# Kernel optimization log

Measured on AMD Instinct MI355X. Metric: run time of the kernel, lower is better.

Reference implementation:

```python
import jax, jax.numpy as jnp
import numpy as np

N = 20000
E = 320000
IN_FEAT = 256
HID = 256
OUT_FEAT = 128


def setup_inputs() -> dict:
    key = jax.random.key(0)
    ks = jax.random.split(key, 10)
    inp = {
        "x": jax.random.normal(ks[0], (N, IN_FEAT), dtype=jnp.float32),
        "edge_src": jax.random.randint(ks[1], (E,), 0, N, dtype=jnp.int32),
        "edge_dst": jax.random.randint(ks[2], (E,), 0, N, dtype=jnp.int32),
        "edge_w": jax.random.uniform(ks[3], (E,), dtype=jnp.float32),
        # params (Linear weights stored as [out, in], torch convention)
        "W_emb": jax.random.normal(ks[4], (HID, IN_FEAT), dtype=jnp.float32) / np.sqrt(IN_FEAT),
        "W_gc1": jax.random.normal(ks[5], (HID, 2 * HID), dtype=jnp.float32) / np.sqrt(2 * HID),
        "b_gc1": jnp.zeros((HID,), dtype=jnp.float32),
        "W_gc2": jax.random.normal(ks[6], (HID, 2 * HID), dtype=jnp.float32) / np.sqrt(2 * HID),
        "b_gc2": jnp.zeros((HID,), dtype=jnp.float32),
        "W_fc": jax.random.normal(ks[7], (OUT_FEAT, HID), dtype=jnp.float32) / np.sqrt(HID),
    }
    return inp


def reference(x, edge_src, edge_dst, edge_w, W_emb, W_gc1, b_gc1, W_gc2, b_gc2, W_fc):
    n = x.shape[0]

    def adj_mul(h):
        msgs = h[edge_src] * edge_w[:, None]           # [E, hid]
        return jax.ops.segment_sum(msgs, edge_dst, num_segments=n)

    def gconv(h, W, b):
        cat = jnp.concatenate([h, adj_mul(h)], axis=1)  # [N, 2*hid]
        return cat @ W.T + b

    h = x @ W_emb.T                                    # embedding (no bias)
    h = h + jax.nn.relu(gconv(h, W_gc1, b_gc1))        # residual (dropout = eval identity)
    h = h + jax.nn.relu(gconv(h, W_gc2, b_gc2))
    out = h @ W_fc.T                                   # fc_last (no bias)
    out = out / jnp.sqrt(jnp.sum(out * out, axis=1, keepdims=True))
    return out
```

## Files before the change

kernel.cpp:

```cpp
#include <hip/hip_runtime.h>
#include <math.h>

#define N_NODES 20000
#define E_EDGES 320000
#define HID 256
#define OUT_FEAT 128
#define MPAD 20224
#define CAP 64

#define BM 128
#define BN 128
#define BK 64
#define LSTR 72

typedef __attribute__((ext_vector_type(8))) __bf16 bf16x8;
typedef __attribute__((ext_vector_type(4))) float floatx4;


__global__ void zero_kernel(int* __restrict__ counts) {
    int i = blockIdx.x * 256 + threadIdx.x;
    if (i < MPAD) counts[i] = 0;
}


#define WBLK 176
#define XBLK 2528
#define EBLK 1250

__global__ void convert_scatter_kernel(
    const float* __restrict__ w0, const float* __restrict__ w1,
    const float* __restrict__ w2, const float* __restrict__ w3,
    __bf16* __restrict__ o0, __bf16* __restrict__ o1,
    __bf16* __restrict__ o2, __bf16* __restrict__ o3,
    const float* __restrict__ x, __bf16* __restrict__ xb,
    const int* __restrict__ src, const int* __restrict__ dst,
    const float* __restrict__ w, int* __restrict__ counts,
    int2* __restrict__ edges) {
    const int b = blockIdx.x;
    if (b < WBLK) {
        const size_t gi = ((size_t)b * 256 + threadIdx.x) * 8;
        const size_t s0 = 65536, s1 = s0 + 131072, s2 = s1 + 131072, s3 = s2 + 32768;
        if (gi >= s3) return;
        const float* srcp; __bf16* dstp; size_t off;
        if (gi < s0)      { srcp = w0; dstp = o0; off = gi; }
        else if (gi < s1) { srcp = w1; dstp = o1; off = gi - s0; }
        else if (gi < s2) { srcp = w2; dstp = o2; off = gi - s1; }
        else              { srcp = w3; dstp = o3; off = gi - s2; }
        float4 v0 = *(const float4*)(srcp + off);
        float4 v1 = *(const float4*)(srcp + off + 4);
        bf16x8 o;
        o[0] = (__bf16)v0.x; o[1] = (__bf16)v0.y; o[2] = (__bf16)v0.z; o[3] = (__bf16)v0.w;
        o[4] = (__bf16)v1.x; o[5] = (__bf16)v1.y; o[6] = (__bf16)v1.z; o[7] = (__bf16)v1.w;
        *(bf16x8*)(dstp + off) = o;
    } else if (b < WBLK + XBLK) {
        const size_t gi = ((size_t)(b - WBLK) * 256 + threadIdx.x) * 8;
        float4 v0 = make_float4(0.f, 0.f, 0.f, 0.f), v1 = v0;
        if (gi < (size_t)N_NODES * HID) {
            v0 = *(const float4*)(x + gi);
            v1 = *(const float4*)(x + gi + 4);
        }
        bf16x8 o;
        o[0] = (__bf16)v0.x; o[1] = (__bf16)v0.y; o[2] = (__bf16)v0.z; o[3] = (__bf16)v0.w;
        o[4] = (__bf16)v1.x; o[5] = (__bf16)v1.y; o[6] = (__bf16)v1.z; o[7] = (__bf16)v1.w;
        *(bf16x8*)(xb + gi) = o;
    } else {
        int e = (b - WBLK - XBLK) * 256 + threadIdx.x;
        if (e < E_EDGES) {
            int d = dst[e];
            int p = atomicAdd(&counts[d], 1);
            edges[(size_t)d * CAP + p] = make_int2(src[e], __float_as_int(w[e]));
        }
    }
}


__global__ __launch_bounds__(256) void aggregate_kernel(
    const __bf16* __restrict__ h, const int* __restrict__ counts,
    const int2* __restrict__ edges, __bf16* __restrict__ agg) {
    const int w = threadIdx.x >> 6, lane = threadIdx.x & 63;
    const int half = lane >> 5, lh = lane & 31;
    const int d = blockIdx.x * 8 + w * 2 + half;
    const size_t base = (size_t)d * CAP;
    const int cnt = counts[d];
    float acc[8];
#pragma unroll
    for (int q = 0; q < 8; q++) acc[q] = 0.f;

    int j = 0;
    for (; j + 16 <= cnt; j += 16) {
        int4 eh[8];
#pragma unroll
        for (int u = 0; u < 8; u++) eh[u] = *(const int4*)(edges + base + j + u * 2);
        bf16x8 hv[16];
#pragma unroll
        for (int u = 0; u < 8; u++) {
            hv[u * 2]     = *(const bf16x8*)(h + (size_t)eh[u].x * HID + lh * 8);
            hv[u * 2 + 1] = *(const bf16x8*)(h + (size_t)eh[u].z * HID + lh * 8);
        }
#pragma unroll
        for (int u = 0; u < 8; u++) {
            float wa = __int_as_float(eh[u].y), wb = __int_as_float(eh[u].w);
#pragma unroll
            for (int q = 0; q < 8; q++) {
                acc[q] = fmaf(wa, (float)hv[u * 2][q], acc[q]);
                acc[q] = fmaf(wb, (float)hv[u * 2 + 1][q], acc[q]);
            }
        }
    }
    for (; j + 8 <= cnt; j += 8) {
        int4 eh[4];
#pragma unroll
        for (int u = 0; u < 4; u++) eh[u] = *(const int4*)(edges + base + j + u * 2);
        bf16x8 hv[8];
#pragma unroll
        for (int u = 0; u < 4; u++) {
            hv[u * 2]     = *(const bf16x8*)(h + (size_t)eh[u].x * HID + lh * 8);
            hv[u * 2 + 1] = *(const bf16x8*)(h + (size_t)eh[u].z * HID + lh * 8);
        }
#pragma unroll
        for (int u = 0; u < 4; u++) {
            float wa = __int_as_float(eh[u].y), wb = __int_as_float(eh[u].w);
#pragma unroll
            for (int q = 0; q < 8; q++) {
                acc[q] = fmaf(wa, (float)hv[u * 2][q], acc[q]);
                acc[q] = fmaf(wb, (float)hv[u * 2 + 1][q], acc[q]);
            }
        }
    }
    for (; j + 2 <= cnt; j += 2) {
        int4 ea = *(const int4*)(edges + base + j);
        bf16x8 h0 = *(const bf16x8*)(h + (size_t)ea.x * HID + lh * 8);
        bf16x8 h1 = *(const bf16x8*)(h + (size_t)ea.z * HID + lh * 8);
        float w0 = __int_as_float(ea.y), w1 = __int_as_float(ea.w);
#pragma unroll
        for (int q = 0; q < 8; q++) {
            acc[q] = fmaf(w0, (float)h0[q], acc[q]);
            acc[q] = fmaf(w1, (float)h1[q], acc[q]);
        }
    }
    if (j < cnt) {
        int2 e0 = edges[base + j];
        bf16x8 h0 = *(const bf16x8*)(h + (size_t)e0.x * HID + lh * 8);
        float w0 = __int_as_float(e0.y);
#pragma unroll
        for (int q = 0; q < 8; q++) acc[q] = fmaf(w0, (float)h0[q], acc[q]);
    }
    bf16x8 o;
#pragma unroll
    for (int q = 0; q < 8; q++) o[q] = (__bf16)acc[q];
    *(bf16x8*)(agg + (size_t)d * HID + lh * 8) = o;
}


template <int KTOT, int EPI>
__global__ __launch_bounds__(256) void gemm_tile_kernel(
    const __bf16* __restrict__ A1,
    const __bf16* __restrict__ A2,
    const __bf16* __restrict__ W,
    const float* __restrict__ bias,
    const __bf16* __restrict__ hres,
    __bf16* __restrict__ outb)
{
    __shared__ __bf16 As[BM * LSTR];
    __shared__ __bf16 Bs[BN * LSTR];
    const int tid = threadIdx.x;
    const int row0 = blockIdx.y * BM;
    const int col0 = blockIdx.x * BN;
    const int wv = tid >> 6, l = tid & 63, lr = l & 15, lq = l >> 4;
    const int wm = wv & 1, wn = wv >> 1;

    floatx4 acc[4][4];
#pragma unroll
    for (int i = 0; i < 4; i++)
#pragma unroll
        for (int j = 0; j < 4; j++) acc[i][j] = (floatx4){0.f, 0.f, 0.f, 0.f};

    const int srow = tid >> 3;
    const int skq = (tid & 7) * 8;

    for (int kc = 0; kc < KTOT; kc += BK) {
        const __bf16* Asrc = (KTOT == 512 && kc >= 256) ? A2 : A1;
        const int ks = (KTOT == 512) ? (kc & 255) : kc;
#pragma unroll
        for (int r = 0; r < 4; r++) {
            int row = r * 32 + srow;
            *(bf16x8*)&As[row * LSTR + skq] =
                *(const bf16x8*)(Asrc + (size_t)(row0 + row) * HID + ks + skq);
        }
#pragma unroll
        for (int r = 0; r < 4; r++) {
            int row = r * 32 + srow;
            *(bf16x8*)&Bs[row * LSTR + skq] =
                *(const bf16x8*)(W + (size_t)(col0 + row) * KTOT + kc + skq);
        }
        __syncthreads();
#pragma unroll
        for (int s = 0; s < 2; s++) {
            bf16x8 af[4], bfr[4];
#pragma unroll
            for (int mt = 0; mt < 4; mt++)
                af[mt] = *(const bf16x8*)&As[(wm * 64 + mt * 16 + lr) * LSTR + s * 32 + lq * 8];
#pragma unroll
            for (int nt = 0; nt < 4; nt++)
                bfr[nt] = *(const bf16x8*)&Bs[(wn * 64 + nt * 16 + lr) * LSTR + s * 32 + lq * 8];
#pragma unroll
            for (int mt = 0; mt < 4; mt++)
#pragma unroll
                for (int nt = 0; nt < 4; nt++)
                    acc[mt][nt] = __builtin_amdgcn_mfma_f32_16x16x32_bf16(af[mt], bfr[nt], acc[mt][nt], 0, 0, 0);
        }
        __syncthreads();
    }

#pragma unroll
    for (int nt = 0; nt < 4; nt++) {
        const int col = col0 + wn * 64 + nt * 16 + lr;
        float b = 0.f;
        if (EPI == 1) b = bias[col];
#pragma unroll
        for (int mt = 0; mt < 4; mt++) {
            const int row = row0 + wm * 64 + mt * 16 + lq * 4;
#pragma unroll
            for (int r = 0; r < 4; r++) {
                float v = acc[mt][nt][r];
                if (EPI == 1) {
                    float res = (float)hres[(size_t)(row + r) * HID + col];
                    v = res + fmaxf(v + b, 0.f);
                }
                outb[(size_t)(row + r) * HID + col] = (__bf16)v;
            }
        }
    }
}


__global__ __launch_bounds__(256) void fc_norm_kernel(
    const __bf16* __restrict__ h,
    const __bf16* __restrict__ W,
    float* __restrict__ out)
{
    const int tid = threadIdx.x;
    const int wv = tid >> 6;
    const int l = tid & 63;
    const int lr = l & 15;
    const int lq = l >> 4;
    const int rowbase = blockIdx.x * 128 + wv * 32;

    floatx4 acc[2][8];
#pragma unroll
    for (int i = 0; i < 2; i++)
#pragma unroll
        for (int j = 0; j < 8; j++) acc[i][j] = (floatx4){0.f, 0.f, 0.f, 0.f};

#pragma unroll
    for (int kt = 0; kt < 256; kt += 32) {
        bf16x8 af[2], bfr[8];
#pragma unroll
        for (int mt = 0; mt < 2; mt++)
            af[mt] = *(const bf16x8*)(h + (size_t)(rowbase + mt * 16 + lr) * 256 + kt + lq * 8);
#pragma unroll
        for (int nt = 0; nt < 8; nt++)
            bfr[nt] = *(const bf16x8*)(W + (size_t)(nt * 16 + lr) * 256 + kt + lq * 8);
#pragma unroll
        for (int mt = 0; mt < 2; mt++)
#pragma unroll
            for (int nt = 0; nt < 8; nt++)
                acc[mt][nt] = __builtin_amdgcn_mfma_f32_16x16x32_bf16(af[mt], bfr[nt], acc[mt][nt], 0, 0, 0);
    }

#pragma unroll
    for (int mt = 0; mt < 2; mt++) {
        float s[4];
#pragma unroll
        for (int r = 0; r < 4; r++) {
            float t = 0.f;
#pragma unroll
            for (int nt = 0; nt < 8; nt++) t = fmaf(acc[mt][nt][r], acc[mt][nt][r], t);
            s[r] = t;
        }
#pragma unroll
        for (int mask = 1; mask <= 8; mask <<= 1) {
#pragma unroll
            for (int r = 0; r < 4; r++) s[r] += __shfl_xor(s[r], mask);
        }
        float inv[4];
#pragma unroll
        for (int r = 0; r < 4; r++) inv[r] = rsqrtf(s[r]);
#pragma unroll
        for (int r = 0; r < 4; r++) {
            int row = rowbase + mt * 16 + lq * 4 + r;
            if (row >= N_NODES) continue;
#pragma unroll
            for (int nt = 0; nt < 8; nt++)
                out[(size_t)row * OUT_FEAT + nt * 16 + lr] = acc[mt][nt][r] * inv[r];
        }
    }
}


extern "C" void kernel_launch(void* const* d_in, const int* in_sizes, int n_in,
                              void* d_out, int out_size, void* d_ws, size_t ws_size,
                              hipStream_t stream) {
    const float* x        = (const float*)d_in[0];
    const int*   edge_src = (const int*)d_in[1];
    const int*   edge_dst = (const int*)d_in[2];
    const float* edge_w   = (const float*)d_in[3];
    const float* W_emb    = (const float*)d_in[4];
    const float* W_gc1    = (const float*)d_in[5];
    const float* b_gc1    = (const float*)d_in[6];
    const float* W_gc2    = (const float*)d_in[7];
    const float* b_gc2    = (const float*)d_in[8];
    const float* W_fc     = (const float*)d_in[9];
    float* out = (float*)d_out;

    char* p = (char*)d_ws;
    const size_t HROW = (size_t)MPAD * HID;
    __bf16* hb0   = (__bf16*)p;             p += HROW * 2;
    __bf16* hb1   = (__bf16*)p;             p += HROW * 2;
    __bf16* aggb  = (__bf16*)p;             p += HROW * 2;
    __bf16* xb    = (__bf16*)p;             p += HROW * 2;
    __bf16* wemb  = (__bf16*)p;             p += 65536 * 2;
    __bf16* w1b   = (__bf16*)p;             p += 131072 * 2;
    __bf16* w2b   = (__bf16*)p;             p += 131072 * 2;
    __bf16* wfcb  = (__bf16*)p;             p += 32768 * 2;
    int2*   edges = (int2*)p;               p += (size_t)N_NODES * CAP * 8;
    int*    counts = (int*)p;               p += (size_t)MPAD * 4;

    zero_kernel<<<MPAD / 256, 256, 0, stream>>>(counts);
    convert_scatter_kernel<<<WBLK + XBLK + EBLK, 256, 0, stream>>>(
        W_emb, W_gc1, W_gc2, W_fc, wemb, w1b, w2b, wfcb,
        x, xb, edge_src, edge_dst, edge_w, counts, edges);

    const dim3 grid_g(HID / BN, MPAD / BM);

    gemm_tile_kernel<256, 0><<<grid_g, 256, 0, stream>>>(xb, nullptr, wemb, nullptr, nullptr, hb0);
    aggregate_kernel<<<N_NODES / 8, 256, 0, stream>>>(hb0, counts, edges, aggb);
    gemm_tile_kernel<512, 1><<<grid_g, 256, 0, stream>>>(hb0, aggb, w1b, b_gc1, hb0, hb1);
    aggregate_kernel<<<N_NODES / 8, 256, 0, stream>>>(hb1, counts, edges, aggb);
    gemm_tile_kernel<512, 1><<<grid_g, 256, 0, stream>>>(hb1, aggb, w2b, b_gc2, hb1, hb0);
    fc_norm_kernel<<<MPAD / 128, 256, 0, stream>>>(hb0, wfcb, out);
}
```

Baseline: 214.5 us.

## Fuse x conversion into embedding GEMM and pad edge lists for uniform aggregation

Removes the separate fp32-to-bf16 conversion of x and its intermediate buffer by converting on the fly while loading the A tile of the embedding GEMM. The aggregate kernel drops its tail loops and always processes 16-edge chunks, relying on a memset that zeros the padded edge slots so extra entries contribute zero weight. The memset adds about 10 MB of writes, and padding causes wasted gathers of row 0.

```diff
diff --git a/kernel.cpp b/kernel.cpp
--- a/kernel.cpp
+++ b/kernel.cpp
@@ -17,14 +17,7 @@
 typedef __attribute__((ext_vector_type(4))) float floatx4;
 
 
-__global__ void zero_kernel(int* __restrict__ counts) {
-    int i = blockIdx.x * 256 + threadIdx.x;
-    if (i < MPAD) counts[i] = 0;
-}
-
-
 #define WBLK 176
-#define XBLK 2528
 #define EBLK 1250
 
 __global__ void convert_scatter_kernel(
@@ -32,7 +25,6 @@
     const float* __restrict__ w2, const float* __restrict__ w3,
     __bf16* __restrict__ o0, __bf16* __restrict__ o1,
     __bf16* __restrict__ o2, __bf16* __restrict__ o3,
-    const float* __restrict__ x, __bf16* __restrict__ xb,
     const int* __restrict__ src, const int* __restrict__ dst,
     const float* __restrict__ w, int* __restrict__ counts,
     int2* __restrict__ edges) {
@@ -52,19 +44,8 @@
         o[0] = (__bf16)v0.x; o[1] = (__bf16)v0.y; o[2] = (__bf16)v0.z; o[3] = (__bf16)v0.w;
         o[4] = (__bf16)v1.x; o[5] = (__bf16)v1.y; o[6] = (__bf16)v1.z; o[7] = (__bf16)v1.w;
         *(bf16x8*)(dstp + off) = o;
-    } else if (b < WBLK + XBLK) {
-        const size_t gi = ((size_t)(b - WBLK) * 256 + threadIdx.x) * 8;
-        float4 v0 = make_float4(0.f, 0.f, 0.f, 0.f), v1 = v0;
-        if (gi < (size_t)N_NODES * HID) {
-            v0 = *(const float4*)(x + gi);
-            v1 = *(const float4*)(x + gi + 4);
-        }
-        bf16x8 o;
-        o[0] = (__bf16)v0.x; o[1] = (__bf16)v0.y; o[2] = (__bf16)v0.z; o[3] = (__bf16)v0.w;
-        o[4] = (__bf16)v1.x; o[5] = (__bf16)v1.y; o[6] = (__bf16)v1.z; o[7] = (__bf16)v1.w;
-        *(bf16x8*)(xb + gi) = o;
     } else {
-        int e = (b - WBLK - XBLK) * 256 + threadIdx.x;
+        int e = (b - WBLK) * 256 + threadIdx.x;
         if (e < E_EDGES) {
             int d = dst[e];
             int p = atomicAdd(&counts[d], 1);
@@ -81,16 +62,16 @@
     const int half = lane >> 5, lh = lane & 31;
     const int d = blockIdx.x * 8 + w * 2 + half;
     const size_t base = (size_t)d * CAP;
-    const int cnt = counts[d];
+    const int iters = (counts[d] + 15) >> 4;
     float acc[8];
 #pragma unroll
     for (int q = 0; q < 8; q++) acc[q] = 0.f;
 
-    int j = 0;
-    for (; j + 16 <= cnt; j += 16) {
+    for (int it = 0; it < iters; ++it) {
+        const int2* ep = edges + base + it * 16;
         int4 eh[8];
 #pragma unroll
-        for (int u = 0; u < 8; u++) eh[u] = *(const int4*)(edges + base + j + u * 2);
+        for (int u = 0; u < 8; u++) eh[u] = *(const int4*)(ep + u * 2);
         bf16x8 hv[16];
 #pragma unroll
         for (int u = 0; u < 8; u++) {
@@ -107,44 +88,6 @@
             }
         }
     }
-    for (; j + 8 <= cnt; j += 8) {
-        int4 eh[4];
-#pragma unroll
-        for (int u = 0; u < 4; u++) eh[u] = *(const int4*)(edges + base + j + u * 2);
-        bf16x8 hv[8];
-#pragma unroll
-        for (int u = 0; u < 4; u++) {
-            hv[u * 2]     = *(const bf16x8*)(h + (size_t)eh[u].x * HID + lh * 8);
-            hv[u * 2 + 1] = *(const bf16x8*)(h + (size_t)eh[u].z * HID + lh * 8);
-        }
-#pragma unroll
-        for (int u = 0; u < 4; u++) {
-            float wa = __int_as_float(eh[u].y), wb = __int_as_float(eh[u].w);
-#pragma unroll
-            for (int q = 0; q < 8; q++) {
-                acc[q] = fmaf(wa, (float)hv[u * 2][q], acc[q]);
-                acc[q] = fmaf(wb, (float)hv[u * 2 + 1][q], acc[q]);
-            }
-        }
-    }
-    for (; j + 2 <= cnt; j += 2) {
-        int4 ea = *(const int4*)(edges + base + j);
-        bf16x8 h0 = *(const bf16x8*)(h + (size_t)ea.x * HID + lh * 8);
-        bf16x8 h1 = *(const bf16x8*)(h + (size_t)ea.z * HID + lh * 8);
-        float w0 = __int_as_float(ea.y), w1 = __int_as_float(ea.w);
-#pragma unroll
-        for (int q = 0; q < 8; q++) {
-            acc[q] = fmaf(w0, (float)h0[q], acc[q]);
-            acc[q] = fmaf(w1, (float)h1[q], acc[q]);
-        }
-    }
-    if (j < cnt) {
-        int2 e0 = edges[base + j];
-        bf16x8 h0 = *(const bf16x8*)(h + (size_t)e0.x * HID + lh * 8);
-        float w0 = __int_as_float(e0.y);
-#pragma unroll
-        for (int q = 0; q < 8; q++) acc[q] = fmaf(w0, (float)h0[q], acc[q]);
-    }
     bf16x8 o;
 #pragma unroll
     for (int q = 0; q < 8; q++) o[q] = (__bf16)acc[q];
@@ -152,9 +95,10 @@
 }
 
 
-template <int KTOT, int EPI>
+template <int KTOT, int EPI, bool F32A>
 __global__ __launch_bounds__(256) void gemm_tile_kernel(
     const __bf16* __restrict__ A1,
+    const float* __restrict__ A1f,
     const __bf16* __restrict__ A2,
     const __bf16* __restrict__ W,
     const float* __restrict__ bias,
@@ -179,13 +123,31 @@
     const int skq = (tid & 7) * 8;
 
     for (int kc = 0; kc < KTOT; kc += BK) {
-        const __bf16* Asrc = (KTOT == 512 && kc >= 256) ? A2 : A1;
-        const int ks = (KTOT == 512) ? (kc & 255) : kc;
-#pragma unroll
-        for (int r = 0; r < 4; r++) {
-            int row = r * 32 + srow;
-            *(bf16x8*)&As[row * LSTR + skq] =
-                *(const bf16x8*)(Asrc + (size_t)(row0 + row) * HID + ks + skq);
+        if (F32A) {
+#pragma unroll
+            for (int r = 0; r < 4; r++) {
+                int row = r * 32 + srow;
+                int grow = row0 + row;
+                float4 v0 = make_float4(0.f, 0.f, 0.f, 0.f), v1 = v0;
+                if (grow < N_NODES) {
+                    const float* xp = A1f + (size_t)grow * HID + kc + skq;
+                    v0 = *(const float4*)xp;
+                    v1 = *(const float4*)(xp + 4);
+                }
+                bf16x8 o;
+                o[0] = (__bf16)v0.x; o[1] = (__bf16)v0.y; o[2] = (__bf16)v0.z; o[3] = (__bf16)v0.w;
+                o[4] = (__bf16)v1.x; o[5] = (__bf16)v1.y; o[6] = (__bf16)v1.z; o[7] = (__bf16)v1.w;
+                *(bf16x8*)&As[row * LSTR + skq] = o;
+            }
+        } else {
+            const __bf16* Asrc = (KTOT == 512 && kc >= 256) ? A2 : A1;
+            const int ks = (KTOT == 512) ? (kc & 255) : kc;
+#pragma unroll
+            for (int r = 0; r < 4; r++) {
+                int row = r * 32 + srow;
+                *(bf16x8*)&As[row * LSTR + skq] =
+                    *(const bf16x8*)(Asrc + (size_t)(row0 + row) * HID + ks + skq);
+            }
         }
 #pragma unroll
         for (int r = 0; r < 4; r++) {
@@ -318,7 +280,6 @@
     __bf16* hb0   = (__bf16*)p;             p += HROW * 2;
     __bf16* hb1   = (__bf16*)p;             p += HROW * 2;
     __bf16* aggb  = (__bf16*)p;             p += HROW * 2;
-    __bf16* xb    = (__bf16*)p;             p += HROW * 2;
     __bf16* wemb  = (__bf16*)p;             p += 65536 * 2;
     __bf16* w1b   = (__bf16*)p;             p += 131072 * 2;
     __bf16* w2b   = (__bf16*)p;             p += 131072 * 2;
@@ -326,17 +287,22 @@
     int2*   edges = (int2*)p;               p += (size_t)N_NODES * CAP * 8;
     int*    counts = (int*)p;               p += (size_t)MPAD * 4;
 
-    zero_kernel<<<MPAD / 256, 256, 0, stream>>>(counts);
-    convert_scatter_kernel<<<WBLK + XBLK + EBLK, 256, 0, stream>>>(
+    hipMemsetAsync(counts, 0, (size_t)MPAD * 4, stream);
+    hipMemsetAsync(edges, 0, (size_t)N_NODES * CAP * 8, stream);
+
+    convert_scatter_kernel<<<WBLK + EBLK, 256, 0, stream>>>(
         W_emb, W_gc1, W_gc2, W_fc, wemb, w1b, w2b, wfcb,
-        x, xb, edge_src, edge_dst, edge_w, counts, edges);
+        edge_src, edge_dst, edge_w, counts, edges);
 
     const dim3 grid_g(HID / BN, MPAD / BM);
 
-    gemm_tile_kernel<256, 0><<<grid_g, 256, 0, stream>>>(xb, nullptr, wemb, nullptr, nullptr, hb0);
+    gemm_tile_kernel<256, 0, true><<<grid_g, 256, 0, stream>>>(
+        nullptr, x, nullptr, wemb, nullptr, nullptr, hb0);
     aggregate_kernel<<<N_NODES / 8, 256, 0, stream>>>(hb0, counts, edges, aggb);
-    gemm_tile_kernel<512, 1><<<grid_g, 256, 0, stream>>>(hb0, aggb, w1b, b_gc1, hb0, hb1);
+    gemm_tile_kernel<512, 1, false><<<grid_g, 256, 0, stream>>>(
+        hb0, nullptr, aggb, w1b, b_gc1, hb0, hb1);
     aggregate_kernel<<<N_NODES / 8, 256, 0, stream>>>(hb1, counts, edges, aggb);
-    gemm_tile_kernel<512, 1><<<grid_g, 256, 0, stream>>>(hb1, aggb, w2b, b_gc2, hb1, hb0);
+    gemm_tile_kernel<512, 1, false><<<grid_g, 256, 0, stream>>>(
+        hb1, nullptr, aggb, w2b, b_gc2, hb1, hb0);
     fc_norm_kernel<<<MPAD / 128, 256, 0, stream>>>(hb0, wfcb, out);
 }
```

Result: faster. 208.5 us (-2.8%).
